# Kernel tuning notes

Hardware: AMD Instinct MI355X
Metric: run time of the kernel (lower is better)

## Reference

```python
import math
import jax, jax.numpy as jnp
import numpy as np

WIDTH = 512
F_TOT = 1024          # min(2*width, 2048)
F_CHUNK = 128
RHO = 0.25
SPECTRAL_SCALE = 0.8
ES_BETA = 6.0
TAU = 0.001
EPS = 1e-8
LN_EPS = 1e-5
N_TOKENS = 4096


def setup_inputs() -> dict:
    key = jax.random.key(0)
    ks = jax.random.split(key, 4)
    x = jax.random.normal(ks[0], (N_TOKENS, WIDTH), dtype=jnp.float32)
    # freq init: linspace(-pi, pi, F) repeated across width
    freq = jnp.tile(jnp.linspace(-math.pi, math.pi, F_TOT, dtype=jnp.float32)[:, None], (1, WIDTH))
    alpha = jax.random.normal(ks[1], (F_TOT, WIDTH), dtype=jnp.float32) * 0.01
    gate = jnp.ones((F_TOT, WIDTH), dtype=jnp.float32) * 0.01
    ln_gamma = jnp.ones((WIDTH,), dtype=jnp.float32)
    ln_beta = jnp.zeros((WIDTH,), dtype=jnp.float32)
    # torch Linear default init: U(-1/sqrt(in), 1/sqrt(in))
    bound = 1.0 / math.sqrt(WIDTH)
    w_loc = jax.random.uniform(ks[2], (WIDTH, WIDTH), dtype=jnp.float32, minval=-bound, maxval=bound)
    b_loc = jax.random.uniform(ks[3], (WIDTH,), dtype=jnp.float32, minval=-bound, maxval=bound)
    return {"x": x, "freq": freq, "alpha": alpha, "gate": gate,
            "ln_gamma": ln_gamma, "ln_beta": ln_beta, "w_loc": w_loc, "b_loc": b_loc}


def reference(x, freq, alpha, gate, ln_gamma, ln_beta, w_loc, b_loc):
    # LayerNorm
    mu = jnp.mean(x, axis=-1, keepdims=True)
    var = jnp.mean((x - mu) ** 2, axis=-1, keepdims=True)
    x_n = (x - mu) / jnp.sqrt(var + LN_EPS) * ln_gamma + ln_beta

    # local branch: Linear -> GELU (exact erf, torch default)
    h_local = jax.nn.gelu(x_n @ w_loc.T + b_loc, approximate=False)

    # spectral weights
    f = freq * SPECTRAL_SCALE
    denom = jax.lax.stop_gradient(jnp.max(jnp.abs(f)))  # .detach().abs().amax()
    safe = jnp.where(denom < 1e-8, 1.0, denom)
    win = jnp.where(denom < 1e-8, jnp.ones_like(f), jnp.exp(-ES_BETA * (f / safe) ** 2))
    raw = alpha * gate
    thr_w = jnp.sign(raw) * jax.nn.relu(jnp.abs(raw) - TAU) * win

    # chunked sin basis expansion, accumulated with lax.scan
    n_chunks = F_TOT // F_CHUNK
    f_r = f.reshape(n_chunks, F_CHUNK, WIDTH)
    t_r = thr_w.reshape(n_chunks, F_CHUNK, WIDTH)

    def body(acc, ft):
        fc, tc = ft  # [C, W] each
        basis = jnp.sin(x_n[:, None, :] * fc[None, :, :])  # [N, C, W]
        return acc + jnp.einsum('ncw,cw->nw', basis, tc), None

    h_spec, _ = jax.lax.scan(jax.checkpoint(body), jnp.zeros_like(x_n), (f_r, t_r))

    # RMS normalize over width
    rms = jnp.sqrt(jnp.mean(h_spec ** 2, axis=1, keepdims=True) + EPS)
    h_spec = h_spec / rms
    return h_local + RHO * h_spec
```

## Files before the change

kernel.cpp:

```cpp
#include <hip/hip_runtime.h>
#include <hip/hip_bf16.h>
#include <math.h>

#define N_TOK 4096
#define W 512
#define F_TOT 1024
#define FW (F_TOT * W)

#define OFF_PARTIAL 0
#define OFF_NNZ     4096
#define OFF_XN      8192
#define OFF_WB      4202496
#define OFF_E       4726784
#define OFF_T       6823936
#define OFF_C       8921088

typedef __attribute__((ext_vector_type(8))) short bf16x8;
typedef __attribute__((ext_vector_type(4))) short bf16x4;
typedef __attribute__((ext_vector_type(4))) float f32x4;

__global__ __launch_bounds__(256) void ln_prep(
    const float* __restrict__ x, const float* __restrict__ freq,
    const float* __restrict__ gamma, const float* __restrict__ beta,
    const float* __restrict__ wloc, __hip_bfloat16* __restrict__ xn,
    __hip_bfloat16* __restrict__ wb, float* __restrict__ partial,
    unsigned* __restrict__ nnz) {
  const int b = blockIdx.x, t = threadIdx.x;
  const int wv = t >> 6, lane = t & 63;
  if (b < 1024) {
    const int row = b * 4 + wv;
    const float4* xr = (const float4*)(x + row * W);
    const float4 p0 = xr[lane * 2];
    const float4 p1 = xr[lane * 2 + 1];
    float s  = p0.x + p0.y + p0.z + p0.w + p1.x + p1.y + p1.z + p1.w;
    float ss = p0.x*p0.x + p0.y*p0.y + p0.z*p0.z + p0.w*p0.w
             + p1.x*p1.x + p1.y*p1.y + p1.z*p1.z + p1.w*p1.w;
#pragma unroll
    for (int m = 32; m > 0; m >>= 1) {
      s  += __shfl_xor(s, m);
      ss += __shfl_xor(ss, m);
    }
    const float mu = s * (1.0f / W);
    const float var = ss * (1.0f / W) - mu * mu;
    const float rstd = rsqrtf(var + 1e-5f);
    const float4 g0 = ((const float4*)gamma)[lane * 2];
    const float4 g1 = ((const float4*)gamma)[lane * 2 + 1];
    const float4 be0 = ((const float4*)beta)[lane * 2];
    const float4 be1 = ((const float4*)beta)[lane * 2 + 1];
    alignas(16) __hip_bfloat16 o[8];
    o[0] = __float2bfloat16((p0.x - mu) * rstd * g0.x + be0.x);
    o[1] = __float2bfloat16((p0.y - mu) * rstd * g0.y + be0.y);
    o[2] = __float2bfloat16((p0.z - mu) * rstd * g0.z + be0.z);
    o[3] = __float2bfloat16((p0.w - mu) * rstd * g0.w + be0.w);
    o[4] = __float2bfloat16((p1.x - mu) * rstd * g1.x + be1.x);
    o[5] = __float2bfloat16((p1.y - mu) * rstd * g1.y + be1.y);
    o[6] = __float2bfloat16((p1.z - mu) * rstd * g1.z + be1.z);
    o[7] = __float2bfloat16((p1.w - mu) * rstd * g1.w + be1.w);
    *(bf16x8*)(xn + row * W + lane * 8) = *(const bf16x8*)o;
  } else if (b < 1280) {
    const int b2 = b - 1024;
    const float4* fp = (const float4*)(freq + b2 * 2048 + wv * 512);
    const float4 q0 = fp[lane * 2];
    const float4 q1 = fp[lane * 2 + 1];
    float mx = fmaxf(fmaxf(fmaxf(fabsf(q0.x), fabsf(q0.y)), fmaxf(fabsf(q0.z), fabsf(q0.w))),
                     fmaxf(fmaxf(fabsf(q1.x), fabsf(q1.y)), fmaxf(fabsf(q1.z), fabsf(q1.w))));
#pragma unroll
    for (int m = 32; m > 0; m >>= 1) mx = fmaxf(mx, __shfl_xor(mx, m));
    if (lane == 0) partial[b2 * 4 + wv] = mx;
    if (b == 1024 && t == 0) *nnz = 0u;
  } else {
    const int i4 = ((b - 1280) * 256 + t);
    const float4 v = ((const float4*)wloc)[i4];
    alignas(8) __hip_bfloat16 o[4];
    o[0] = __float2bfloat16(v.x);
    o[1] = __float2bfloat16(v.y);
    o[2] = __float2bfloat16(v.z);
    o[3] = __float2bfloat16(v.w);
    *(bf16x4*)(wb + i4 * 4) = *(const bf16x4*)o;
  }
}

__global__ __launch_bounds__(64) void gemm_thr(
    const __hip_bfloat16* __restrict__ xn, const __hip_bfloat16* __restrict__ wb,
    const float* __restrict__ bias, float* __restrict__ out,
    const float* __restrict__ freq, const float* __restrict__ alpha,
    const float* __restrict__ gate, const float* __restrict__ partial,
    unsigned* __restrict__ nnz, unsigned* __restrict__ eArr,
    float* __restrict__ tArr, float* __restrict__ cArr) {
  const int bid = blockIdx.x;
  const int lane = threadIdx.x;

  if (bid < 512) {
    float mx = 0.0f;
#pragma unroll
    for (int j = 0; j < 16; ++j) mx = fmaxf(mx, partial[lane + j * 64]);
#pragma unroll
    for (int m = 32; m > 0; m >>= 1) mx = fmaxf(mx, __shfl_xor(mx, m));
    const float denom = mx * 0.8f;
    const bool tiny = denom < 1e-8f;
    const float inv = tiny ? 0.0f : (1.0f / denom);
    const int base = bid * 1024 + lane;
#pragma unroll
    for (int j = 0; j < 16; ++j) {
      const int e = base + j * 64;
      const float f = freq[e] * 0.8f;
      const float raw = alpha[e] * gate[e];
      const float v = fabsf(raw) - 1e-3f;
      if (v > 0.0f) {
        const float r = f * inv;
        const float win = tiny ? 1.0f : expf(-6.0f * r * r);
        const float tw = copysignf(v, raw) * win;
        const unsigned idx = atomicAdd(nnz, 1u);
        eArr[idx] = (unsigned)e;
        tArr[idx] = tw;
        cArr[idx] = f;
      }
    }
    return;
  }

  const int bid2 = bid - 512;
  const int tm = bid2 >> 3;
  const int tn = bid2 & 7;
  const int m = lane & 15;
  const int q = lane >> 4;
  const short* A = (const short*)xn + (tm * 16 + m) * W + q * 8;
  const short* B = (const short*)wb + (tn * 64 + m) * W + q * 8;
  f32x4 acc[4] = {};

  bf16x8 a_cur = *(const bf16x8*)A;
  bf16x8 b_cur[4];
#pragma unroll
  for (int j = 0; j < 4; ++j) b_cur[j] = *(const bf16x8*)(B + (j * 16) * W);

#pragma unroll
  for (int k0 = 0; k0 < W; k0 += 32) {
    bf16x8 a_nxt;
    bf16x8 b_nxt[4];
    if (k0 + 32 < W) {
      a_nxt = *(const bf16x8*)(A + k0 + 32);
#pragma unroll
      for (int j = 0; j < 4; ++j)
        b_nxt[j] = *(const bf16x8*)(B + (j * 16) * W + k0 + 32);
    }
#pragma unroll
    for (int j = 0; j < 4; ++j)
      acc[j] = __builtin_amdgcn_mfma_f32_16x16x32_bf16(a_cur, b_cur[j], acc[j], 0, 0, 0);
    a_cur = a_nxt;
#pragma unroll
    for (int j = 0; j < 4; ++j) b_cur[j] = b_nxt[j];
  }

#pragma unroll
  for (int j = 0; j < 4; ++j) {
    const int col = tn * 64 + j * 16 + m;
    const float bv = bias[col];
#pragma unroll
    for (int r = 0; r < 4; ++r) {
      const int row = tm * 16 + q * 4 + r;
      const float v = acc[j][r] + bv;
      const float g = 0.5f * v * (1.0f + erff(v * 0.70710678118654752f));
      out[row * W + col] = g;
    }
  }
}

__global__ __launch_bounds__(64) void spectral_final(
    const __hip_bfloat16* __restrict__ xn, const unsigned* __restrict__ nnz,
    const unsigned* __restrict__ eArr, const float* __restrict__ tArr,
    const float* __restrict__ cArr, float* __restrict__ out) {
  const unsigned cnt = *nnz;
  if (cnt == 0) return;
  const int lane = threadIdx.x;
  for (int n = blockIdx.x; n < N_TOK; n += gridDim.x) {
    float xv[8], h[8];
#pragma unroll
    for (int j = 0; j < 8; ++j) {
      xv[j] = __bfloat162float(xn[n * W + lane + j * 64]);
      h[j] = 0.0f;
    }
    for (unsigned i = 0; i < cnt; ++i) {
      const unsigned e = eArr[i];
      const int we = (int)(e & (W - 1));
      if ((we & 63) == lane) {
        const int j = we >> 6;
        h[j] += tArr[i] * sinf(xv[j] * cArr[i]);
      }
    }
    float ss = 0.0f;
#pragma unroll
    for (int j = 0; j < 8; ++j) ss += h[j] * h[j];
#pragma unroll
    for (int m = 32; m > 0; m >>= 1) ss += __shfl_xor(ss, m);
    const float rms = sqrtf(ss * (1.0f / W) + 1e-8f);
    const float sc = 0.25f / rms;
#pragma unroll
    for (int j = 0; j < 8; ++j) out[n * W + lane + j * 64] += sc * h[j];
  }
}

extern "C" void kernel_launch(void* const* d_in, const int* in_sizes, int n_in,
                              void* d_out, int out_size, void* d_ws, size_t ws_size,
                              hipStream_t stream) {
  const float* x     = (const float*)d_in[0];
  const float* freq  = (const float*)d_in[1];
  const float* alpha = (const float*)d_in[2];
  const float* gate  = (const float*)d_in[3];
  const float* gamma = (const float*)d_in[4];
  const float* beta  = (const float*)d_in[5];
  const float* wloc  = (const float*)d_in[6];
  const float* bloc  = (const float*)d_in[7];
  float* out = (float*)d_out;

  char* ws = (char*)d_ws;
  float* partial       = (float*)(ws + OFF_PARTIAL);
  unsigned* nnz        = (unsigned*)(ws + OFF_NNZ);
  __hip_bfloat16* xn   = (__hip_bfloat16*)(ws + OFF_XN);
  __hip_bfloat16* wb   = (__hip_bfloat16*)(ws + OFF_WB);
  unsigned* eArr       = (unsigned*)(ws + OFF_E);
  float* tArr          = (float*)(ws + OFF_T);
  float* cArr          = (float*)(ws + OFF_C);

  hipLaunchKernelGGL(ln_prep, dim3(1536), dim3(256), 0, stream,
                     x, freq, gamma, beta, wloc, xn, wb, partial, nnz);
  hipLaunchKernelGGL(gemm_thr, dim3(2560), dim3(64), 0, stream,
                     xn, wb, bloc, out, freq, alpha, gate, partial,
                     nnz, eArr, tArr, cArr);
  hipLaunchKernelGGL(spectral_final, dim3(512), dim3(64), 0, stream,
                     xn, nnz, eArr, tArr, cArr, out);
}
```

Measured before the change: 100.1 us.

## Fuse LayerNorm, weight conversion and GEMM into one kernel with per-group compaction

Merges the three-kernel pipeline into two. LayerNorm is computed per 64-row tile and the weights are converted to bf16 inside the GEMM blocks through swizzled LDS, so the xn and bf16 weight intermediates are no longer written to global memory. Sparse-weight compaction now uses per-wave ballot/popcount into fixed per-group slots instead of a global atomic counter. The window exponent and the LayerNorm recompute move into spectral_final, which now walks 512 group counts. The cost is redundant LayerNorm and weight conversion per tile, and extra per-token work in the spectral pass if many entries survive the threshold.

```diff
diff --git a/kernel.cpp b/kernel.cpp
--- a/kernel.cpp
+++ b/kernel.cpp
@@ -7,148 +7,149 @@
 #define F_TOT 1024
 #define FW (F_TOT * W)
 
-#define OFF_PARTIAL 0
-#define OFF_NNZ     4096
-#define OFF_XN      8192
-#define OFF_WB      4202496
-#define OFF_E       4726784
-#define OFF_T       6823936
-#define OFF_C       8921088
+#define OFF_CNT     0
+#define OFF_PARTIAL 4096
+#define OFF_E       8192
+#define OFF_T       (8192 + FW * 4)
+#define OFF_C       (8192 + FW * 8)
 
 typedef __attribute__((ext_vector_type(8))) short bf16x8;
-typedef __attribute__((ext_vector_type(4))) short bf16x4;
 typedef __attribute__((ext_vector_type(4))) float f32x4;
 
-__global__ __launch_bounds__(256) void ln_prep(
+__device__ __forceinline__ bf16x8 pack8(float a0, float a1, float a2, float a3,
+                                        float a4, float a5, float a6, float a7) {
+  alignas(16) __hip_bfloat16 o[8];
+  o[0] = __float2bfloat16(a0); o[1] = __float2bfloat16(a1);
+  o[2] = __float2bfloat16(a2); o[3] = __float2bfloat16(a3);
+  o[4] = __float2bfloat16(a4); o[5] = __float2bfloat16(a5);
+  o[6] = __float2bfloat16(a6); o[7] = __float2bfloat16(a7);
+  return *(const bf16x8*)o;
+}
+
+__global__ __launch_bounds__(256) void fused_main(
     const float* __restrict__ x, const float* __restrict__ freq,
+    const float* __restrict__ alpha, const float* __restrict__ gate,
     const float* __restrict__ gamma, const float* __restrict__ beta,
-    const float* __restrict__ wloc, __hip_bfloat16* __restrict__ xn,
-    __hip_bfloat16* __restrict__ wb, float* __restrict__ partial,
-    unsigned* __restrict__ nnz) {
-  const int b = blockIdx.x, t = threadIdx.x;
+    const float* __restrict__ wloc, const float* __restrict__ bias,
+    float* __restrict__ out, unsigned* __restrict__ cnt,
+    float* __restrict__ partial, unsigned* __restrict__ eArr,
+    float* __restrict__ tArr, float* __restrict__ cArr) {
+  __shared__ alignas(128) char lds_raw[65536];
+  const int bid = blockIdx.x, t = threadIdx.x;
   const int wv = t >> 6, lane = t & 63;
-  if (b < 1024) {
-    const int row = b * 4 + wv;
-    const float4* xr = (const float4*)(x + row * W);
+
+  if (bid < 128) {
+    const int g = bid * 4 + wv;
+    const int base = g * 1024;
+    unsigned c = 0;
+    float mx = 0.0f;
+#pragma unroll
+    for (int j = 0; j < 16; ++j) {
+      const int e = base + j * 64 + lane;
+      const float f = freq[e] * 0.8f;
+      const float raw = alpha[e] * gate[e];
+      const float v = fabsf(raw) - 1e-3f;
+      mx = fmaxf(mx, fabsf(f));
+      const bool pred = v > 0.0f;
+      const unsigned long long mk = __ballot(pred);
+      if (pred) {
+        const unsigned idx = base + c + (unsigned)__popcll(mk & ((1ull << lane) - 1ull));
+        eArr[idx] = (unsigned)e;
+        tArr[idx] = copysignf(v, raw);
+        cArr[idx] = f;
+      }
+      c += (unsigned)__popcll(mk);
+    }
+#pragma unroll
+    for (int mm = 32; mm > 0; mm >>= 1) mx = fmaxf(mx, __shfl_xor(mx, mm));
+    if (lane == 0) { cnt[g] = c; partial[g] = mx; }
+    return;
+  }
+
+  const int bid2 = bid - 128;
+  const int tm = bid2 >> 3;
+  const int tn = bid2 & 7;
+  const int m = lane & 15, q = lane >> 4;
+
+  const float4 g0 = ((const float4*)gamma)[lane * 2];
+  const float4 g1 = ((const float4*)gamma)[lane * 2 + 1];
+  const float4 be0 = ((const float4*)beta)[lane * 2];
+  const float4 be1 = ((const float4*)beta)[lane * 2 + 1];
+
+  for (int rr = 0; rr < 16; ++rr) {
+    const int lrow = wv * 16 + rr;
+    const float4* xr = (const float4*)(x + (tm * 64 + lrow) * W);
     const float4 p0 = xr[lane * 2];
     const float4 p1 = xr[lane * 2 + 1];
     float s  = p0.x + p0.y + p0.z + p0.w + p1.x + p1.y + p1.z + p1.w;
     float ss = p0.x*p0.x + p0.y*p0.y + p0.z*p0.z + p0.w*p0.w
              + p1.x*p1.x + p1.y*p1.y + p1.z*p1.z + p1.w*p1.w;
 #pragma unroll
-    for (int m = 32; m > 0; m >>= 1) {
-      s  += __shfl_xor(s, m);
-      ss += __shfl_xor(ss, m);
+    for (int mm = 32; mm > 0; mm >>= 1) {
+      s  += __shfl_xor(s, mm);
+      ss += __shfl_xor(ss, mm);
     }
     const float mu = s * (1.0f / W);
-    const float var = ss * (1.0f / W) - mu * mu;
-    const float rstd = rsqrtf(var + 1e-5f);
-    const float4 g0 = ((const float4*)gamma)[lane * 2];
-    const float4 g1 = ((const float4*)gamma)[lane * 2 + 1];
-    const float4 be0 = ((const float4*)beta)[lane * 2];
-    const float4 be1 = ((const float4*)beta)[lane * 2 + 1];
-    alignas(16) __hip_bfloat16 o[8];
-    o[0] = __float2bfloat16((p0.x - mu) * rstd * g0.x + be0.x);
-    o[1] = __float2bfloat16((p0.y - mu) * rstd * g0.y + be0.y);
-    o[2] = __float2bfloat16((p0.z - mu) * rstd * g0.z + be0.z);
-    o[3] = __float2bfloat16((p0.w - mu) * rstd * g0.w + be0.w);
-    o[4] = __float2bfloat16((p1.x - mu) * rstd * g1.x + be1.x);
-    o[5] = __float2bfloat16((p1.y - mu) * rstd * g1.y + be1.y);
-    o[6] = __float2bfloat16((p1.z - mu) * rstd * g1.z + be1.z);
-    o[7] = __float2bfloat16((p1.w - mu) * rstd * g1.w + be1.w);
-    *(bf16x8*)(xn + row * W + lane * 8) = *(const bf16x8*)o;
-  } else if (b < 1280) {
-    const int b2 = b - 1024;
-    const float4* fp = (const float4*)(freq + b2 * 2048 + wv * 512);
-    const float4 q0 = fp[lane * 2];
-    const float4 q1 = fp[lane * 2 + 1];
-    float mx = fmaxf(fmaxf(fmaxf(fabsf(q0.x), fabsf(q0.y)), fmaxf(fabsf(q0.z), fabsf(q0.w))),
-                     fmaxf(fmaxf(fabsf(q1.x), fabsf(q1.y)), fmaxf(fabsf(q1.z), fabsf(q1.w))));
-#pragma unroll
-    for (int m = 32; m > 0; m >>= 1) mx = fmaxf(mx, __shfl_xor(mx, m));
-    if (lane == 0) partial[b2 * 4 + wv] = mx;
-    if (b == 1024 && t == 0) *nnz = 0u;
-  } else {
-    const int i4 = ((b - 1280) * 256 + t);
-    const float4 v = ((const float4*)wloc)[i4];
-    alignas(8) __hip_bfloat16 o[4];
-    o[0] = __float2bfloat16(v.x);
-    o[1] = __float2bfloat16(v.y);
-    o[2] = __float2bfloat16(v.z);
-    o[3] = __float2bfloat16(v.w);
-    *(bf16x4*)(wb + i4 * 4) = *(const bf16x4*)o;
-  }
-}
-
-__global__ __launch_bounds__(64) void gemm_thr(
-    const __hip_bfloat16* __restrict__ xn, const __hip_bfloat16* __restrict__ wb,
-    const float* __restrict__ bias, float* __restrict__ out,
-    const float* __restrict__ freq, const float* __restrict__ alpha,
-    const float* __restrict__ gate, const float* __restrict__ partial,
-    unsigned* __restrict__ nnz, unsigned* __restrict__ eArr,
-    float* __restrict__ tArr, float* __restrict__ cArr) {
-  const int bid = blockIdx.x;
-  const int lane = threadIdx.x;
-
-  if (bid < 512) {
-    float mx = 0.0f;
-#pragma unroll
-    for (int j = 0; j < 16; ++j) mx = fmaxf(mx, partial[lane + j * 64]);
-#pragma unroll
-    for (int m = 32; m > 0; m >>= 1) mx = fmaxf(mx, __shfl_xor(mx, m));
-    const float denom = mx * 0.8f;
-    const bool tiny = denom < 1e-8f;
-    const float inv = tiny ? 0.0f : (1.0f / denom);
-    const int base = bid * 1024 + lane;
-#pragma unroll
-    for (int j = 0; j < 16; ++j) {
-      const int e = base + j * 64;
-      const float f = freq[e] * 0.8f;
-      const float raw = alpha[e] * gate[e];
-      const float v = fabsf(raw) - 1e-3f;
-      if (v > 0.0f) {
-        const float r = f * inv;
-        const float win = tiny ? 1.0f : expf(-6.0f * r * r);
-        const float tw = copysignf(v, raw) * win;
-        const unsigned idx = atomicAdd(nnz, 1u);
-        eArr[idx] = (unsigned)e;
-        tArr[idx] = tw;
-        cArr[idx] = f;
+    const float rstd = rsqrtf(ss * (1.0f / W) - mu * mu + 1e-5f);
+    const bf16x8 o = pack8((p0.x - mu) * rstd * g0.x + be0.x,
+                           (p0.y - mu) * rstd * g0.y + be0.y,
+                           (p0.z - mu) * rstd * g0.z + be0.z,
+                           (p0.w - mu) * rstd * g0.w + be0.w,
+                           (p1.x - mu) * rstd * g1.x + be1.x,
+                           (p1.y - mu) * rstd * g1.y + be1.y,
+                           (p1.z - mu) * rstd * g1.z + be1.z,
+                           (p1.w - mu) * rstd * g1.w + be1.w);
+    *(bf16x8*)(lds_raw + lrow * 1024 + ((lane * 16) ^ ((lrow & 7) << 4))) = o;
+  }
+  __syncthreads();
+
+  bf16x8 a[16];
+  {
+    const int lrow = wv * 16 + m;
+    const char* rbase = lds_raw + lrow * 1024;
+    const int swz = (lrow & 7) << 4;
+#pragma unroll
+    for (int kk = 0; kk < 16; ++kk)
+      a[kk] = *(const bf16x8*)(rbase + (((kk * 32 + q * 8) * 2) ^ swz));
+  }
+  __syncthreads();
+
+  {
+    const float* wbase = wloc + (tn * 64) * W;
+#pragma unroll
+    for (int i = 0; i < 16; ++i) {
+      const int n = i * 4 + wv;
+      const float4* wr = (const float4*)(wbase + n * W);
+      const float4 u0 = wr[lane * 2];
+      const float4 u1 = wr[lane * 2 + 1];
+      const bf16x8 o = pack8(u0.x, u0.y, u0.z, u0.w, u1.x, u1.y, u1.z, u1.w);
+      *(bf16x8*)(lds_raw + n * 1024 + ((lane * 16) ^ ((n & 7) << 4))) = o;
+    }
+  }
+  __syncthreads();
+
+  f32x4 acc[4] = {};
+  bf16x8 bc[4], bn[4];
+#pragma unroll
+  for (int j = 0; j < 4; ++j) {
+    const int n = j * 16 + m;
+    bc[j] = *(const bf16x8*)(lds_raw + n * 1024 + (((q * 8) * 2) ^ ((n & 7) << 4)));
+  }
+#pragma unroll
+  for (int kk = 0; kk < 16; ++kk) {
+    if (kk < 15) {
+#pragma unroll
+      for (int j = 0; j < 4; ++j) {
+        const int n = j * 16 + m;
+        const int kb = ((kk + 1) * 32 + q * 8) * 2;
+        bn[j] = *(const bf16x8*)(lds_raw + n * 1024 + (kb ^ ((n & 7) << 4)));
       }
     }
-    return;
-  }
-
-  const int bid2 = bid - 512;
-  const int tm = bid2 >> 3;
-  const int tn = bid2 & 7;
-  const int m = lane & 15;
-  const int q = lane >> 4;
-  const short* A = (const short*)xn + (tm * 16 + m) * W + q * 8;
-  const short* B = (const short*)wb + (tn * 64 + m) * W + q * 8;
-  f32x4 acc[4] = {};
-
-  bf16x8 a_cur = *(const bf16x8*)A;
-  bf16x8 b_cur[4];
-#pragma unroll
-  for (int j = 0; j < 4; ++j) b_cur[j] = *(const bf16x8*)(B + (j * 16) * W);
-
-#pragma unroll
-  for (int k0 = 0; k0 < W; k0 += 32) {
-    bf16x8 a_nxt;
-    bf16x8 b_nxt[4];
-    if (k0 + 32 < W) {
-      a_nxt = *(const bf16x8*)(A + k0 + 32);
-#pragma unroll
-      for (int j = 0; j < 4; ++j)
-        b_nxt[j] = *(const bf16x8*)(B + (j * 16) * W + k0 + 32);
-    }
 #pragma unroll
     for (int j = 0; j < 4; ++j)
-      acc[j] = __builtin_amdgcn_mfma_f32_16x16x32_bf16(a_cur, b_cur[j], acc[j], 0, 0, 0);
-    a_cur = a_nxt;
-#pragma unroll
-    for (int j = 0; j < 4; ++j) b_cur[j] = b_nxt[j];
+      acc[j] = __builtin_amdgcn_mfma_f32_16x16x32_bf16(a[kk], bc[j], acc[j], 0, 0, 0);
+#pragma unroll
+    for (int j = 0; j < 4; ++j) bc[j] = bn[j];
   }
 
 #pragma unroll
@@ -157,43 +158,82 @@
     const float bv = bias[col];
 #pragma unroll
     for (int r = 0; r < 4; ++r) {
-      const int row = tm * 16 + q * 4 + r;
+      const int row = tm * 64 + wv * 16 + q * 4 + r;
       const float v = acc[j][r] + bv;
-      const float g = 0.5f * v * (1.0f + erff(v * 0.70710678118654752f));
-      out[row * W + col] = g;
+      out[row * W + col] = 0.5f * v * (1.0f + erff(v * 0.70710678118654752f));
     }
   }
 }
 
 __global__ __launch_bounds__(64) void spectral_final(
-    const __hip_bfloat16* __restrict__ xn, const unsigned* __restrict__ nnz,
-    const unsigned* __restrict__ eArr, const float* __restrict__ tArr,
-    const float* __restrict__ cArr, float* __restrict__ out) {
-  const unsigned cnt = *nnz;
-  if (cnt == 0) return;
+    const float* __restrict__ x, const float* __restrict__ gamma,
+    const float* __restrict__ beta, const unsigned* __restrict__ cnt,
+    const float* __restrict__ partial, const unsigned* __restrict__ eArr,
+    const float* __restrict__ tArr, const float* __restrict__ cArr,
+    float* __restrict__ out) {
   const int lane = threadIdx.x;
+  unsigned tot = 0;
+#pragma unroll
+  for (int j = 0; j < 8; ++j) tot += cnt[lane + j * 64];
+#pragma unroll
+  for (int mm = 32; mm > 0; mm >>= 1) tot += __shfl_xor(tot, mm);
+  if (tot == 0) return;
+
+  float mx = 0.0f;
+#pragma unroll
+  for (int j = 0; j < 8; ++j) mx = fmaxf(mx, partial[lane + j * 64]);
+#pragma unroll
+  for (int mm = 32; mm > 0; mm >>= 1) mx = fmaxf(mx, __shfl_xor(mx, mm));
+  const bool tiny = mx < 1e-8f;
+  const float inv = tiny ? 0.0f : 1.0f / mx;
+
+  float gm[8], bt[8];
+#pragma unroll
+  for (int j = 0; j < 8; ++j) {
+    gm[j] = gamma[lane + j * 64];
+    bt[j] = beta[lane + j * 64];
+  }
+
   for (int n = blockIdx.x; n < N_TOK; n += gridDim.x) {
-    float xv[8], h[8];
+    float xv[8], s = 0.0f, ss = 0.0f;
 #pragma unroll
     for (int j = 0; j < 8; ++j) {
-      xv[j] = __bfloat162float(xn[n * W + lane + j * 64]);
-      h[j] = 0.0f;
-    }
-    for (unsigned i = 0; i < cnt; ++i) {
-      const unsigned e = eArr[i];
-      const int we = (int)(e & (W - 1));
-      if ((we & 63) == lane) {
-        const int j = we >> 6;
-        h[j] += tArr[i] * sinf(xv[j] * cArr[i]);
+      xv[j] = x[n * W + lane + j * 64];
+      s += xv[j];
+      ss += xv[j] * xv[j];
+    }
+#pragma unroll
+    for (int mm = 32; mm > 0; mm >>= 1) {
+      s += __shfl_xor(s, mm);
+      ss += __shfl_xor(ss, mm);
+    }
+    const float mu = s * (1.0f / W);
+    const float rstd = rsqrtf(ss * (1.0f / W) - mu * mu + 1e-5f);
+#pragma unroll
+    for (int j = 0; j < 8; ++j) xv[j] = (xv[j] - mu) * rstd * gm[j] + bt[j];
+
+    float h[8] = {0, 0, 0, 0, 0, 0, 0, 0};
+    for (int g = 0; g < 512; ++g) {
+      const unsigned cs = cnt[g];
+      const unsigned b0 = (unsigned)g * 1024u;
+      for (unsigned i = 0; i < cs; ++i) {
+        const unsigned e = eArr[b0 + i];
+        const int we = (int)(e & (W - 1));
+        if ((we & 63) == lane) {
+          const int j = we >> 6;
+          const float f = cArr[b0 + i];
+          const float r = f * inv;
+          const float win = tiny ? 1.0f : expf(-6.0f * r * r);
+          h[j] += tArr[b0 + i] * win * sinf(xv[j] * f);
+        }
       }
     }
-    float ss = 0.0f;
-#pragma unroll
-    for (int j = 0; j < 8; ++j) ss += h[j] * h[j];
-#pragma unroll
-    for (int m = 32; m > 0; m >>= 1) ss += __shfl_xor(ss, m);
-    const float rms = sqrtf(ss * (1.0f / W) + 1e-8f);
-    const float sc = 0.25f / rms;
+    float s2 = 0.0f;
+#pragma unroll
+    for (int j = 0; j < 8; ++j) s2 += h[j] * h[j];
+#pragma unroll
+    for (int mm = 32; mm > 0; mm >>= 1) s2 += __shfl_xor(s2, mm);
+    const float sc = 0.25f / sqrtf(s2 * (1.0f / W) + 1e-8f);
 #pragma unroll
     for (int j = 0; j < 8; ++j) out[n * W + lane + j * 64] += sc * h[j];
   }
@@ -213,19 +253,15 @@
   float* out = (float*)d_out;
 
   char* ws = (char*)d_ws;
-  float* partial       = (float*)(ws + OFF_PARTIAL);
-  unsigned* nnz        = (unsigned*)(ws + OFF_NNZ);
-  __hip_bfloat16* xn   = (__hip_bfloat16*)(ws + OFF_XN);
-  __hip_bfloat16* wb   = (__hip_bfloat16*)(ws + OFF_WB);
-  unsigned* eArr       = (unsigned*)(ws + OFF_E);
-  float* tArr          = (float*)(ws + OFF_T);
-  float* cArr          = (float*)(ws + OFF_C);
-
-  hipLaunchKernelGGL(ln_prep, dim3(1536), dim3(256), 0, stream,
-                     x, freq, gamma, beta, wloc, xn, wb, partial, nnz);
-  hipLaunchKernelGGL(gemm_thr, dim3(2560), dim3(64), 0, stream,
-                     xn, wb, bloc, out, freq, alpha, gate, partial,
-                     nnz, eArr, tArr, cArr);
+  unsigned* cnt  = (unsigned*)(ws + OFF_CNT);
+  float* partial = (float*)(ws + OFF_PARTIAL);
+  unsigned* eArr = (unsigned*)(ws + OFF_E);
+  float* tArr    = (float*)(ws + OFF_T);
+  float* cArr    = (float*)(ws + OFF_C);
+
+  hipLaunchKernelGGL(fused_main, dim3(640), dim3(256), 0, stream,
+                     x, freq, alpha, gate, gamma, beta, wloc, bloc,
+                     out, cnt, partial, eArr, tArr, cArr);
   hipLaunchKernelGGL(spectral_final, dim3(512), dim3(64), 0, stream,
-                     xn, nnz, eArr, tArr, cArr, out);
-}
+                     x, gamma, beta, cnt, partial, eArr, tArr, cArr, out);
+}
```

Measured after the change: 99.46 us. Within noise of the previous version (-0.6%).
